# Kernel tuning notes

Measured on AMD Instinct MI355X. Metric: run time of the kernel, lower is better.

The kernel has to match this reference:

```python
import jax, jax.numpy as jnp
import numpy as np

MAX_SEQ_LEN = 128
H = 512
B = 256
S = 128
VOCAB = MAX_SEQ_LEN + 2
SOS = MAX_SEQ_LEN  # start token index in embedding table


def _lstm_cell(x, h, c, w_ih, w_hh, b):
    # PyTorch gate order: i, f, g, o
    z = x @ w_ih.T + h @ w_hh.T + b
    i, f, g, o = jnp.split(z, 4, axis=-1)
    c = jax.nn.sigmoid(f) * c + jax.nn.sigmoid(i) * jnp.tanh(g)
    h = jax.nn.sigmoid(o) * jnp.tanh(c)
    return h, c


def _run_layer(xs, w_ih, w_hh, b):
    nb = xs.shape[1]
    h0 = jnp.zeros((nb, H), xs.dtype)

    def step(carry, x):
        h, c = carry
        h, c = _lstm_cell(x, h, c, w_ih, w_hh, b)
        return (h, c), h

    (hT, cT), ys = jax.lax.scan(step, (h0, h0), xs)
    return ys, hT, cT


def _forward(l2_features, enc, dec, emb, fc1_w, fc1_b, fc2_w, fc2_b, fc3_w, mlp):
    xs = jnp.transpose(l2_features, (1, 0, 2))  # [S,B,F]
    hs, cs = [], []
    for (w_ih, w_hh, b) in enc:  # 3-layer encoder LSTM
        xs, hT, cT = _run_layer(xs, w_ih, w_hh, b)
        hs.append(hT)
        cs.append(cT)
    enc_outs = xs  # [S,B,H]
    h_stack = jnp.stack(hs)  # [3,B,H]
    c_stack = jnp.stack(cs)
    ot = enc_outs @ fc2_w.T + fc2_b  # [S,B,256], loop-invariant
    w1, b1, w2, b2, w3, b3 = mlp
    (dw_ih0, dw_hh0, db0), (dw_ih1, dw_hh1, db1), (dw_ih2, dw_hh2, db2) = dec
    nb = l2_features.shape[0]
    tok0 = jnp.full((nb,), SOS, dtype=jnp.int32)
    ctx0 = jnp.zeros((nb, H), l2_features.dtype)

    def dec_step(carry, _):
        h, c, ctx, tok = carry
        # dropout is identity in eval mode
        x = jnp.concatenate([emb[tok], ctx], axis=1)  # [B, 2H]
        h0, c0 = _lstm_cell(x, h[0], c[0], dw_ih0, dw_hh0, db0)
        h1, c1 = _lstm_cell(h0, h[1], c[1], dw_ih1, dw_hh1, db1)
        h2, c2 = _lstm_cell(h1, h[2], c[2], dw_ih2, dw_hh2, db2)
        ht = h2 @ fc1_w.T + fc1_b  # [B,256]
        scores = jnp.tanh(ot + ht[None]) @ fc3_w[0]  # [S,B]
        w = jax.nn.softmax(scores, axis=0)  # softmax over encoder time (dim 0)
        new_ctx = jnp.einsum('sb,sbd->bd', w, enc_outs)  # [B,H]
        hdd = jax.nn.relu(jnp.concatenate([h2, new_ctx], axis=1) @ w1.T + b1)
        hdd = jax.nn.relu(hdd @ w2.T + b2)
        out = hdd @ w3.T + b3  # [B, MAX_SEQ_LEN]
        new_tok = jnp.argmax(out, axis=-1).astype(jnp.int32)
        new_carry = (jnp.stack([h0, h1, h2]), jnp.stack([c0, c1, c2]), new_ctx, new_tok)
        return new_carry, out

    _, outs = jax.lax.scan(dec_step, (h_stack, c_stack, ctx0, tok0), None, length=MAX_SEQ_LEN)
    return outs  # [MAX_SEQ_LEN, B, MAX_SEQ_LEN]


def setup_inputs() -> dict:
    key = jax.random.key(0)
    ks = iter(jax.random.split(key, 40))

    def p(shape):
        return jax.random.normal(next(ks), shape, dtype=jnp.float32) * 0.05

    d = {"l2_features": jax.random.normal(next(ks), (B, S, MAX_SEQ_LEN), dtype=jnp.float32)}
    d["enc_w_ih0"] = p((4 * H, MAX_SEQ_LEN)); d["enc_w_hh0"] = p((4 * H, H)); d["enc_b0"] = p((4 * H,))
    d["enc_w_ih1"] = p((4 * H, H)); d["enc_w_hh1"] = p((4 * H, H)); d["enc_b1"] = p((4 * H,))
    d["enc_w_ih2"] = p((4 * H, H)); d["enc_w_hh2"] = p((4 * H, H)); d["enc_b2"] = p((4 * H,))
    d["dec_w_ih0"] = p((4 * H, 2 * H)); d["dec_w_hh0"] = p((4 * H, H)); d["dec_b0"] = p((4 * H,))
    d["dec_w_ih1"] = p((4 * H, H)); d["dec_w_hh1"] = p((4 * H, H)); d["dec_b1"] = p((4 * H,))
    d["dec_w_ih2"] = p((4 * H, H)); d["dec_w_hh2"] = p((4 * H, H)); d["dec_b2"] = p((4 * H,))
    d["emb"] = p((VOCAB, H))
    d["fc1_w"] = p((256, H)); d["fc1_b"] = p((256,))
    d["fc2_w"] = p((256, H)); d["fc2_b"] = p((256,))
    d["fc3_w"] = p((1, 256))
    d["mlp_w1"] = p((512, 1024)); d["mlp_b1"] = p((512,))
    d["mlp_w2"] = p((256, 512)); d["mlp_b2"] = p((256,))
    d["mlp_w3"] = p((MAX_SEQ_LEN, 256)); d["mlp_b3"] = p((MAX_SEQ_LEN,))
    return d


def reference(l2_features, enc_w_ih0, enc_w_hh0, enc_b0, enc_w_ih1, enc_w_hh1, enc_b1,
              enc_w_ih2, enc_w_hh2, enc_b2, dec_w_ih0, dec_w_hh0, dec_b0,
              dec_w_ih1, dec_w_hh1, dec_b1, dec_w_ih2, dec_w_hh2, dec_b2,
              emb, fc1_w, fc1_b, fc2_w, fc2_b, fc3_w,
              mlp_w1, mlp_b1, mlp_w2, mlp_b2, mlp_w3, mlp_b3):
    enc = ((enc_w_ih0, enc_w_hh0, enc_b0), (enc_w_ih1, enc_w_hh1, enc_b1), (enc_w_ih2, enc_w_hh2, enc_b2))
    dec = ((dec_w_ih0, dec_w_hh0, dec_b0), (dec_w_ih1, dec_w_hh1, dec_b1), (dec_w_ih2, dec_w_hh2, dec_b2))
    mlp = (mlp_w1, mlp_b1, mlp_w2, mlp_b2, mlp_w3, mlp_b3)
    return _forward(l2_features, enc, dec, emb, fc1_w, fc1_b, fc2_w, fc2_b, fc3_w, mlp)
```

## Files before the change

### kernel.cpp

```cpp
#include <hip/hip_runtime.h>

#define BB 256
#define SS 128
#define FDIM 128
#define HH 512
#define H4 2048
#define TDEC 128
#define SOS_TOK 128

typedef short short8 __attribute__((ext_vector_type(8)));
typedef float f32x4 __attribute__((ext_vector_type(4)));

__device__ __forceinline__ float sigf(float x){ return 1.0f/(1.0f+__expf(-x)); }
__device__ __forceinline__ float tanh_f(float x){ return 1.0f - 2.0f/(__expf(2.0f*x)+1.0f); }

__device__ __forceinline__ void split2(float x, unsigned& h, unsigned& m){
    union { float f; unsigned u; } a; a.f = x;
    h = (a.u + 0x7fffu + ((a.u>>16)&1u)) >> 16;
    union { unsigned u; float f; } hf; hf.u = h << 16;
    float r1 = x - hf.f;
    union { float f; unsigned u; } b; b.f = r1;
    m = (b.u + 0x7fffu + ((b.u>>16)&1u)) >> 16;
}

__device__ __forceinline__ void splitw8(float4 v, uint2& H, uint2& M){
    unsigned h0,m0,h1,m1,h2,m2,h3,m3;
    split2(v.x,h0,m0); split2(v.y,h1,m1); split2(v.z,h2,m2); split2(v.w,h3,m3);
    H.x = h0 | (h1<<16); H.y = h2 | (h3<<16);
    M.x = m0 | (m1<<16); M.y = m2 | (m3<<16);
}

__global__ void split_w(const float* __restrict__ srcA, int KA,
                        const float* __restrict__ srcB, int KB, int ilv,
                        unsigned short* __restrict__ ph, unsigned short* __restrict__ pm,
                        int N){
    int k = blockIdx.x*128 + threadIdx.x;
    int n = blockIdx.y;
    int K = KA + KB;
    if (k >= K) return;
    int row = ilv ? ((n&3)*512 + (n>>2)) : n;
    float w = (k < KA) ? srcA[(size_t)row*KA + k] : srcB[(size_t)row*KB + (k-KA)];
    unsigned h,m; split2(w,h,m);
    size_t off = (size_t)(k>>5)*((size_t)N*32) + (size_t)n*32
               + ((((k>>3)&3) ^ (n&3))<<3) + (k&7);
    ph[off]=(unsigned short)h; pm[off]=(unsigned short)m;
}

__global__ void repack_b(float* __restrict__ dst, const float* __restrict__ src){
    int id = blockIdx.x*256 + threadIdx.x;
    if (id >= 2048) return;
    int g = id & 3, q = id >> 2;
    dst[id] = src[g*512 + q];
}

__global__ void init_tok(int* __restrict__ tok){ tok[threadIdx.x] = SOS_TOK; }

#define MM3(AH,AM,BH,BM,C) \
  C = __builtin_amdgcn_mfma_f32_16x16x32_bf16(AH,BH,C,0,0,0); \
  C = __builtin_amdgcn_mfma_f32_16x16x32_bf16(AH,BM,C,0,0,0); \
  C = __builtin_amdgcn_mfma_f32_16x16x32_bf16(AM,BH,C,0,0,0);

template<int MODE>
__global__ __launch_bounds__(256) void mg(
    const float* __restrict__ A0, long a0B, long a0T,
    const float* __restrict__ A1, const float* __restrict__ A2,
    const int* __restrict__ tok, int ksh,
    const unsigned short* __restrict__ Wh, const unsigned short* __restrict__ Wm,
    int Nld, int Kc,
    const float* __restrict__ bias, int relu,
    float* __restrict__ out, long oB, long oT,
    const float* __restrict__ xz, float* __restrict__ c_io, float* __restrict__ seqo)
{
    __shared__ __align__(16) unsigned short sA[2][2][2048];
    __shared__ __align__(16) unsigned short sW[2][2][2048];
    const int tid = threadIdx.x;
    const int row0 = blockIdx.y * 64, col0 = blockIdx.x * 64;
    const int nk = Kc >> 5;

    f32x4 acc[2][2];
    acc[0][0] = (f32x4){0.f,0.f,0.f,0.f}; acc[0][1] = (f32x4){0.f,0.f,0.f,0.f};
    acc[1][0] = (f32x4){0.f,0.f,0.f,0.f}; acc[1][1] = (f32x4){0.f,0.f,0.f,0.f};

    const int sr = tid >> 2, q4 = tid & 3;
    const int gr = row0 + sr;
    long ro0;
    if (tok){ int rr = tok[gr & 255]; ro0 = (long)rr * a0B; }
    else ro0 = (long)(gr & 255)*a0B + (long)(gr >> 8)*a0T;
    const long ro1 = (long)gr * 512;
    const size_t wbase = (size_t)col0*32 + (size_t)tid*8;
    const int swz = sr & 3;
    const int b0 = sr*32 + (q4 & 1)*4;
    const int p0s = ((q4>>1) ^ swz) << 3;
    const int p1s = ((2 + (q4>>1)) ^ swz) << 3;

    float4 va0, va1; uint4 vw0, vw1;

    auto issue = [&](int kt){
        int kg = kt*32;
        int seg = kg >> ksh;
        const float* sp = (seg==0)? A0 : ((seg==1)? A1 : A2);
        long ro = (seg==0)? ro0 : ro1;
        int ko = kg & ((1<<ksh)-1);
        const float* p = sp + ro + ko + q4*4;
        va0 = *(const float4*)p;
        va1 = *(const float4*)(p + 16);
        size_t wi = (size_t)(kg>>5)*((size_t)Nld*32) + wbase;
        vw0 = *(const uint4*)(Wh + wi);
        vw1 = *(const uint4*)(Wm + wi);
    };
    auto commit = [&](int buf){
        uint2 H,M;
        splitw8(va0,H,M);
        *(uint2*)&sA[buf][0][b0 + p0s] = H;
        *(uint2*)&sA[buf][1][b0 + p0s] = M;
        splitw8(va1,H,M);
        *(uint2*)&sA[buf][0][b0 + p1s] = H;
        *(uint2*)&sA[buf][1][b0 + p1s] = M;
        *(uint4*)&sW[buf][0][tid*8] = vw0;
        *(uint4*)&sW[buf][1][tid*8] = vw1;
    };

    const int wid = tid >> 6, lane = tid & 63;
    const int wy = wid >> 1, wx = wid & 1;
    const int l15 = lane & 15, l4 = lane >> 4;
    const int offA = (wy*32 + l15)*32 + ((l4 ^ (l15&3))<<3);
    const int offB = (wx*32 + l15)*32 + ((l4 ^ (l15&3))<<3);

    auto compute = [&](int buf){
        short8 a0h = *(const short8*)&sA[buf][0][offA];
        short8 a0m = *(const short8*)&sA[buf][1][offA];
        short8 a1h = *(const short8*)&sA[buf][0][offA+512];
        short8 a1m = *(const short8*)&sA[buf][1][offA+512];
        short8 b0h = *(const short8*)&sW[buf][0][offB];
        short8 b0m = *(const short8*)&sW[buf][1][offB];
        short8 b1h = *(const short8*)&sW[buf][0][offB+512];
        short8 b1m = *(const short8*)&sW[buf][1][offB+512];
        MM3(a0h,a0m,b0h,b0m,acc[0][0])
        MM3(a0h,a0m,b1h,b1m,acc[0][1])
        MM3(a1h,a1m,b0h,b0m,acc[1][0])
        MM3(a1h,a1m,b1h,b1m,acc[1][1])
    };

    issue(0);
    commit(0);
    __syncthreads();
    int buf = 0;
    for (int kt=0; kt<nk; ++kt){
        bool more = (kt+1 < nk);
        if (more) issue(kt+1);
        compute(buf);
        if (more) commit(buf^1);
        __syncthreads();
        buf ^= 1;
    }

    if (MODE == 0){
        #pragma unroll
        for (int fa=0; fa<2; fa++){
            #pragma unroll
            for (int fb=0; fb<2; fb++){
                int gc = col0 + wx*32 + fb*16 + l15;
                float bv = bias ? bias[gc] : 0.0f;
                #pragma unroll
                for (int i=0;i<4;i++){
                    int r = row0 + wy*32 + fa*16 + l4*4 + i;
                    float v = acc[fa][fb][i] + bv;
                    if (relu) v = fmaxf(v, 0.0f);
                    out[(size_t)(r&255)*oB + (size_t)(r>>8)*oT + gc] = v;
                }
            }
        }
    } else {
        #pragma unroll
        for (int fa=0; fa<2; fa++){
            #pragma unroll
            for (int fb=0; fb<2; fb++){
                int gc = col0 + wx*32 + fb*16 + l15;
                int q = gc >> 2, g = gc & 3;
                float ab = xz ? 0.0f : bias[gc];
                #pragma unroll
                for (int i=0;i<4;i++){
                    int r = row0 + wy*32 + fa*16 + l4*4 + i;
                    float addv = xz ? xz[(size_t)r*2048 + gc] : ab;
                    float z = acc[fa][fb][i] + addv;
                    float x1 = __shfl_xor(z, 1);
                    float x2 = __shfl_xor(z, 2);
                    float x3 = __shfl_xor(z, 3);
                    float zi = (g==0)?z :(g==1)?x1:(g==2)?x2:x3;
                    float zf = (g==1)?z :(g==0)?x1:(g==3)?x2:x3;
                    float zg = (g==2)?z :(g==3)?x1:(g==0)?x2:x3;
                    float zo = (g==3)?z :(g==2)?x1:(g==1)?x2:x3;
                    float co = c_io[(size_t)r*512 + q];
                    float cn = sigf(zf)*co + sigf(zi)*tanh_f(zg);
                    float hn = sigf(zo)*tanh_f(cn);
                    if (g == 1) c_io[(size_t)r*512 + q] = cn;
                    else if (g == 0) seqo[(size_t)r*512 + q] = hn;
                }
            }
        }
    }
}

__global__ __launch_bounds__(256) void attn_fc1(
    const float* __restrict__ h2,
    const float* __restrict__ fc1w,
    const float* __restrict__ fc1b,
    const float* __restrict__ ot,
    const float* __restrict__ enc,
    const float* __restrict__ fc3,
    float* __restrict__ ctx)
{
    __shared__ float h2s[512], hts[256], f3s[256], wsm[SS];
    const int b = blockIdx.x, tid = threadIdx.x;
    h2s[tid]     = h2[(size_t)b*512 + tid];
    h2s[tid+256] = h2[(size_t)b*512 + tid + 256];
    f3s[tid] = fc3[tid];
    __syncthreads();
    {
        const float4* wr = (const float4*)(fc1w + (size_t)tid*512);
        float s0=0.f, s1=0.f;
        #pragma unroll 4
        for (int k4=0; k4<128; k4+=2){
            float4 w0 = wr[k4], w1 = wr[k4+1];
            float4 hh0 = *(const float4*)&h2s[k4*4];
            float4 hh1 = *(const float4*)&h2s[k4*4+4];
            s0 = fmaf(w0.x,hh0.x,fmaf(w0.y,hh0.y,fmaf(w0.z,hh0.z,fmaf(w0.w,hh0.w,s0))));
            s1 = fmaf(w1.x,hh1.x,fmaf(w1.y,hh1.y,fmaf(w1.z,hh1.z,fmaf(w1.w,hh1.w,s1))));
        }
        hts[tid] = s0 + s1 + fc1b[tid];
    }
    __syncthreads();
    const int wave = tid >> 6, lane = tid & 63;
    const float* otb = ot + (size_t)b*SS*256;
    for (int i=0;i<32;i++){
        int s = wave*32 + i;
        float4 o = *(const float4*)&otb[(size_t)s*256 + lane*4];
        int d0 = lane*4;
        float v = f3s[d0+0]*tanh_f(o.x + hts[d0+0])
                + f3s[d0+1]*tanh_f(o.y + hts[d0+1])
                + f3s[d0+2]*tanh_f(o.z + hts[d0+2])
                + f3s[d0+3]*tanh_f(o.w + hts[d0+3]);
        #pragma unroll
        for (int off=32; off; off>>=1) v += __shfl_xor(v, off);
        if (lane == 0) wsm[s] = v;
    }
    __syncthreads();
    if (tid < 64){
        float v0 = wsm[tid], v1 = wsm[tid+64];
        float m = fmaxf(v0, v1);
        #pragma unroll
        for (int off=32; off; off>>=1) m = fmaxf(m, __shfl_xor(m, off));
        float e0 = __expf(v0 - m), e1 = __expf(v1 - m);
        float ss = e0 + e1;
        #pragma unroll
        for (int off=32; off; off>>=1) ss += __shfl_xor(ss, off);
        float inv = 1.0f/ss;
        wsm[tid] = e0*inv; wsm[tid+64] = e1*inv;
    }
    __syncthreads();
    float a0=0.f, a1=0.f;
    const float* eb = enc + (size_t)b*HH;
    #pragma unroll 8
    for (int s=0;s<SS;s++){
        float w = wsm[s];
        const float* e = eb + (size_t)s*BB*HH;
        a0 = fmaf(w, e[tid],      a0);
        a1 = fmaf(w, e[tid+256],  a1);
    }
    ctx[(size_t)b*HH + tid]      = a0;
    ctx[(size_t)b*HH + tid+256]  = a1;
}

__global__ __launch_bounds__(128) void mlp3_argmax(
    const float* __restrict__ hdd2,
    const float* __restrict__ w3,
    const float* __restrict__ b3,
    float* __restrict__ outp,
    int* __restrict__ tok)
{
    __shared__ float hs[256], lg[128];
    const int b = blockIdx.x, tid = threadIdx.x;
    hs[tid]     = hdd2[(size_t)b*256 + tid];
    hs[tid+128] = hdd2[(size_t)b*256 + tid + 128];
    __syncthreads();
    const float4* wr = (const float4*)(w3 + (size_t)tid*256);
    float s0=0.f, s1=0.f;
    #pragma unroll 4
    for (int k4=0; k4<64; k4+=2){
        float4 w0 = wr[k4], w1 = wr[k4+1];
        float4 h0 = *(const float4*)&hs[k4*4];
        float4 h1 = *(const float4*)&hs[k4*4+4];
        s0 = fmaf(w0.x,h0.x,fmaf(w0.y,h0.y,fmaf(w0.z,h0.z,fmaf(w0.w,h0.w,s0))));
        s1 = fmaf(w1.x,h1.x,fmaf(w1.y,h1.y,fmaf(w1.z,h1.z,fmaf(w1.w,h1.w,s1))));
    }
    float v = s0 + s1 + b3[tid];
    outp[(size_t)b*128 + tid] = v;
    lg[tid] = v;
    __syncthreads();
    if (tid < 64){
        float v0 = lg[tid], v1 = lg[tid+64];
        float bv; int bi;
        if (v1 > v0){ bv = v1; bi = tid+64; } else { bv = v0; bi = tid; }
        #pragma unroll
        for (int off=32; off; off>>=1){
            float ov = __shfl_xor(bv, off);
            int   oi = __shfl_xor(bi, off);
            if (ov > bv || (ov == bv && oi < bi)){ bv = ov; bi = oi; }
        }
        if (tid == 0) tok[b] = bi;
    }
}

extern "C" void kernel_launch(void* const* d_in, const int* in_sizes, int n_in,
                              void* d_out, int out_size, void* d_ws, size_t ws_size,
                              hipStream_t stream)
{
    (void)in_sizes; (void)n_in; (void)out_size;
    const float* l2      = (const float*)d_in[0];
    const float* e_wih[3] = {(const float*)d_in[1],(const float*)d_in[4],(const float*)d_in[7]};
    const float* e_whh[3] = {(const float*)d_in[2],(const float*)d_in[5],(const float*)d_in[8]};
    const float* e_b[3]   = {(const float*)d_in[3],(const float*)d_in[6],(const float*)d_in[9]};
    const float* d_wih[3] = {(const float*)d_in[10],(const float*)d_in[13],(const float*)d_in[16]};
    const float* d_whh[3] = {(const float*)d_in[11],(const float*)d_in[14],(const float*)d_in[17]};
    const float* d_b[3]   = {(const float*)d_in[12],(const float*)d_in[15],(const float*)d_in[18]};
    const float* emb   = (const float*)d_in[19];
    const float* fc1_w = (const float*)d_in[20]; const float* fc1_b = (const float*)d_in[21];
    const float* fc2_w = (const float*)d_in[22]; const float* fc2_b = (const float*)d_in[23];
    const float* fc3_w = (const float*)d_in[24];
    const float* w1 = (const float*)d_in[25]; const float* b1 = (const float*)d_in[26];
    const float* w2 = (const float*)d_in[27]; const float* b2 = (const float*)d_in[28];
    const float* w3 = (const float*)d_in[29]; const float* b3 = (const float*)d_in[30];
    float* out = (float*)d_out;

    float* base = (float*)d_ws;
    size_t off = 0;
    auto alloc = [&](size_t n)->float*{ float* r = base + off; off = (off + n + 63) & ~(size_t)63; return r; };

    struct WSpec { const float* a; int ka; const float* b; int kb; int ilv; int n; };
    WSpec ws[13] = {
        {e_wih[0],128, nullptr,0, 1,2048}, {e_wih[1],512, nullptr,0, 1,2048}, {e_wih[2],512, nullptr,0, 1,2048},
        {e_whh[0],512, nullptr,0, 1,2048}, {e_whh[1],512, nullptr,0, 1,2048}, {e_whh[2],512, nullptr,0, 1,2048},
        {d_wih[0],1024, d_whh[0],512, 1,2048}, {d_wih[1],512, d_whh[1],512, 1,2048}, {d_wih[2],512, d_whh[2],512, 1,2048},
        {fc2_w,512, nullptr,0, 0,256},
        {w1,1024, nullptr,0, 0,512}, {w2,512, nullptr,0, 0,256}, {w3,256, nullptr,0, 0,128}
    };
    unsigned short* wp[13][2];
    for (int i=0;i<13;i++){
        size_t sz = (size_t)(ws[i].ka + ws[i].kb) * ws[i].n;
        float* blk = alloc(sz);
        wp[i][0] = (unsigned short*)blk;
        wp[i][1] = wp[i][0] + sz;
    }
    float* br_e[3]; for (int l=0;l<3;l++) br_e[l] = alloc(2048);
    float* br_d[3]; for (int l=0;l<3;l++) br_d[l] = alloc(2048);

    float* seq   = alloc((size_t)SS*BB*HH);
    float* ot    = alloc((size_t)BB*SS*256);
    float* zbuf  = alloc((size_t)BB*HH);
    float* cbuf[3]; for (int l=0;l<3;l++) cbuf[l] = alloc((size_t)BB*HH);
    float* hbuf[3][2];
    for (int l=0;l<3;l++) for (int p=0;p<2;p++) hbuf[l][p] = alloc((size_t)BB*HH);
    float* ctx  = alloc((size_t)BB*HH);
    float* hdd1 = alloc((size_t)BB*512);
    float* hdd2 = alloc((size_t)BB*256);
    int*   tok  = (int*)alloc(256);

    size_t remain = (ws_size/4 > off) ? (ws_size/4 - off) : 0;
    int CH = 4;
    if      (remain >= (size_t)32*BB*H4) CH = 32;
    else if (remain >= (size_t)16*BB*H4) CH = 16;
    else if (remain >= (size_t) 8*BB*H4) CH = 8;
    float* xz = base + off;

    for (int i=0;i<13;i++){
        int K = ws[i].ka + ws[i].kb;
        hipLaunchKernelGGL(split_w, dim3((K+127)/128, ws[i].n), dim3(128), 0, stream,
                           ws[i].a, ws[i].ka, ws[i].b, ws[i].kb, ws[i].ilv,
                           wp[i][0], wp[i][1], ws[i].n);
    }
    for (int l=0;l<3;l++){
        hipLaunchKernelGGL(repack_b, dim3(8), dim3(256), 0, stream, br_e[l], e_b[l]);
        hipLaunchKernelGGL(repack_b, dim3(8), dim3(256), 0, stream, br_d[l], d_b[l]);
    }
    hipMemsetAsync(zbuf, 0, (size_t)BB*HH*4, stream);
    for (int l=0;l<3;l++) hipMemsetAsync(cbuf[l], 0, (size_t)BB*HH*4, stream);
    hipMemsetAsync(ctx, 0, (size_t)BB*HH*4, stream);

    for (int l=0;l<3;l++){
        const int Kih = (l==0)? FDIM : HH;
        const int nch = SS / CH;
        for (int tc=0; tc<nch; tc++){
            const float* A0; long sB, sT;
            if (l == 0){ A0 = l2 + (size_t)tc*CH*FDIM; sB = (long)SS*FDIM; sT = FDIM; }
            else       { A0 = seq + (size_t)tc*CH*BB*HH; sB = HH; sT = (long)BB*HH; }
            hipLaunchKernelGGL((mg<0>), dim3(32, CH*4), dim3(256), 0, stream,
                A0, sB, sT, (const float*)nullptr, (const float*)nullptr, (const int*)nullptr, 30,
                wp[l][0], wp[l][1], 2048, Kih,
                br_e[l], 0, xz, (long)H4, (long)BB*H4,
                (const float*)nullptr, (float*)nullptr, (float*)nullptr);
            for (int ti=0; ti<CH; ti++){
                int t = tc*CH + ti;
                const float* hp = (t==0) ? zbuf : seq + (size_t)(t-1)*BB*HH;
                hipLaunchKernelGGL((mg<2>), dim3(32, 4), dim3(256), 0, stream,
                    hp, (long)HH, 0L, (const float*)nullptr, (const float*)nullptr, (const int*)nullptr, 30,
                    wp[3+l][0], wp[3+l][1], 2048, HH,
                    (const float*)nullptr, 0, (float*)nullptr, 0L, 0L,
                    xz + (size_t)ti*BB*H4, cbuf[l], seq + (size_t)t*BB*HH);
            }
        }
        hipMemcpyAsync(hbuf[l][0], seq + (size_t)(SS-1)*BB*HH, (size_t)BB*HH*4,
                       hipMemcpyDeviceToDevice, stream);
    }

    hipLaunchKernelGGL((mg<0>), dim3(4, 512), dim3(256), 0, stream,
        seq, (long)HH, (long)BB*HH, (const float*)nullptr, (const float*)nullptr, (const int*)nullptr, 30,
        wp[9][0], wp[9][1], 256, HH,
        fc2_b, 0, ot, (long)SS*256, 256L,
        (const float*)nullptr, (float*)nullptr, (float*)nullptr);

    hipLaunchKernelGGL(init_tok, dim3(1), dim3(256), 0, stream, tok);
    for (int t=0; t<TDEC; t++){
        const int p = t & 1;
        hipLaunchKernelGGL((mg<2>), dim3(32, 4), dim3(256), 0, stream,
            emb, (long)HH, 0L, ctx, hbuf[0][p], tok, 9,
            wp[6][0], wp[6][1], 2048, 3*HH,
            br_d[0], 0, (float*)nullptr, 0L, 0L,
            (const float*)nullptr, cbuf[0], hbuf[0][p^1]);
        hipLaunchKernelGGL((mg<2>), dim3(32, 4), dim3(256), 0, stream,
            hbuf[0][p^1], (long)HH, 0L, hbuf[1][p], (const float*)nullptr, (const int*)nullptr, 9,
            wp[7][0], wp[7][1], 2048, 2*HH,
            br_d[1], 0, (float*)nullptr, 0L, 0L,
            (const float*)nullptr, cbuf[1], hbuf[1][p^1]);
        hipLaunchKernelGGL((mg<2>), dim3(32, 4), dim3(256), 0, stream,
            hbuf[1][p^1], (long)HH, 0L, hbuf[2][p], (const float*)nullptr, (const int*)nullptr, 9,
            wp[8][0], wp[8][1], 2048, 2*HH,
            br_d[2], 0, (float*)nullptr, 0L, 0L,
            (const float*)nullptr, cbuf[2], hbuf[2][p^1]);
        hipLaunchKernelGGL(attn_fc1, dim3(BB), dim3(256), 0, stream,
            hbuf[2][p^1], fc1_w, fc1_b, ot, seq, fc3_w, ctx);
        hipLaunchKernelGGL((mg<0>), dim3(8, 4), dim3(256), 0, stream,
            hbuf[2][p^1], (long)HH, 0L, ctx, (const float*)nullptr, (const int*)nullptr, 9,
            wp[10][0], wp[10][1], 512, 2*HH,
            b1, 1, hdd1, 512L, 0L,
            (const float*)nullptr, (float*)nullptr, (float*)nullptr);
        hipLaunchKernelGGL((mg<0>), dim3(4, 4), dim3(256), 0, stream,
            hdd1, 512L, 0L, (const float*)nullptr, (const float*)nullptr, (const int*)nullptr, 30,
            wp[11][0], wp[11][1], 256, HH,
            b2, 1, hdd2, 256L, 0L,
            (const float*)nullptr, (float*)nullptr, (float*)nullptr);
        hipLaunchKernelGGL(mlp3_argmax, dim3(BB), dim3(128), 0, stream,
            hdd2, w3, b3, out + (size_t)t*BB*128, tok);
    }
}
```

Baseline: 32.81 ms.

## Replace per-step kernel launches with persistent encoder/decoder kernels using grid barriers

Replaces the many per-timestep launches (encoder chunked input GEMMs plus recurrent GEMMs, and seven kernels per decoder step) with two persistent 256-workgroup kernels that synchronise through a global atomic barrier. The encoder runs a wavefront over layers and time so that up to three layers' cells execute concurrently, and it fuses the input and hidden weights into a single K-concatenated GEMM. The decoder moves fc1 onto the split-bf16 MFMA path and runs attention, the MLP and argmax as phases inside one kernel. The goal is to remove launch overhead and serialisation on this latency-bound recurrence. In exchange it depends on all 256 workgroups being co-resident for the spin barrier to avoid deadlock, and many phases leave most workgroups idle.

```diff
diff --git a/kernel.cpp b/kernel.cpp
--- a/kernel.cpp
+++ b/kernel.cpp
@@ -7,9 +7,12 @@
 #define H4 2048
 #define TDEC 128
 #define SOS_TOK 128
+#define NWG 256
+#define SLOT 131072
 
 typedef short short8 __attribute__((ext_vector_type(8)));
 typedef float f32x4 __attribute__((ext_vector_type(4)));
+typedef unsigned short ushort_t;
 
 __device__ __forceinline__ float sigf(float x){ return 1.0f/(1.0f+__expf(-x)); }
 __device__ __forceinline__ float tanh_f(float x){ return 1.0f - 2.0f/(__expf(2.0f*x)+1.0f); }
@@ -32,8 +35,7 @@
 
 __global__ void split_w(const float* __restrict__ srcA, int KA,
                         const float* __restrict__ srcB, int KB, int ilv,
-                        unsigned short* __restrict__ ph, unsigned short* __restrict__ pm,
-                        int N){
+                        ushort_t* __restrict__ ph, ushort_t* __restrict__ pm, int N){
     int k = blockIdx.x*128 + threadIdx.x;
     int n = blockIdx.y;
     int K = KA + KB;
@@ -43,7 +45,7 @@
     unsigned h,m; split2(w,h,m);
     size_t off = (size_t)(k>>5)*((size_t)N*32) + (size_t)n*32
                + ((((k>>3)&3) ^ (n&3))<<3) + (k&7);
-    ph[off]=(unsigned short)h; pm[off]=(unsigned short)m;
+    ph[off]=(ushort_t)h; pm[off]=(ushort_t)m;
 }
 
 __global__ void repack_b(float* __restrict__ dst, const float* __restrict__ src){
@@ -53,58 +55,66 @@
     dst[id] = src[g*512 + q];
 }
 
-__global__ void init_tok(int* __restrict__ tok){ tok[threadIdx.x] = SOS_TOK; }
-
-#define MM3(AH,AM,BH,BM,C) \
-  C = __builtin_amdgcn_mfma_f32_16x16x32_bf16(AH,BH,C,0,0,0); \
-  C = __builtin_amdgcn_mfma_f32_16x16x32_bf16(AH,BM,C,0,0,0); \
-  C = __builtin_amdgcn_mfma_f32_16x16x32_bf16(AM,BH,C,0,0,0);
-
-template<int MODE>
-__global__ __launch_bounds__(256) void mg(
+__global__ void init_misc(int* bar){ if (threadIdx.x < 2) bar[threadIdx.x] = 0; }
+
+__device__ __forceinline__ void gbar(int* bar){
+    __syncthreads();
+    if (threadIdx.x == 0){
+        __threadfence();
+        int g = __hip_atomic_load(&bar[1], __ATOMIC_RELAXED, __HIP_MEMORY_SCOPE_AGENT);
+        int a = __hip_atomic_fetch_add(&bar[0], 1, __ATOMIC_ACQ_REL, __HIP_MEMORY_SCOPE_AGENT);
+        if (a == NWG-1){
+            __hip_atomic_store(&bar[0], 0, __ATOMIC_RELAXED, __HIP_MEMORY_SCOPE_AGENT);
+            __hip_atomic_fetch_add(&bar[1], 1, __ATOMIC_ACQ_REL, __HIP_MEMORY_SCOPE_AGENT);
+        } else {
+            while (__hip_atomic_load(&bar[1], __ATOMIC_ACQUIRE, __HIP_MEMORY_SCOPE_AGENT) == g)
+                __builtin_amdgcn_s_sleep(8);
+        }
+        __threadfence();
+    }
+    __syncthreads();
+}
+
+__device__ __forceinline__ void gtile(
+    ushort_t (&sA)[2][2][2048], ushort_t (&sW)[2][2][2048],
+    int row0, int col0,
     const float* __restrict__ A0, long a0B, long a0T,
     const float* __restrict__ A1, const float* __restrict__ A2,
-    const int* __restrict__ tok, int ksh,
-    const unsigned short* __restrict__ Wh, const unsigned short* __restrict__ Wm,
-    int Nld, int Kc,
-    const float* __restrict__ bias, int relu,
+    const int* __restrict__ tok,
+    int kx1, int kx2, int Kc,
+    const ushort_t* __restrict__ Wh, const ushort_t* __restrict__ Wm, int Nld,
+    const float* __restrict__ bias, int relu, int mode,
     float* __restrict__ out, long oB, long oT,
-    const float* __restrict__ xz, float* __restrict__ c_io, float* __restrict__ seqo)
+    float* __restrict__ c_io, float* __restrict__ seqo)
 {
-    __shared__ __align__(16) unsigned short sA[2][2][2048];
-    __shared__ __align__(16) unsigned short sW[2][2][2048];
     const int tid = threadIdx.x;
-    const int row0 = blockIdx.y * 64, col0 = blockIdx.x * 64;
     const int nk = Kc >> 5;
-
     f32x4 acc[2][2];
-    acc[0][0] = (f32x4){0.f,0.f,0.f,0.f}; acc[0][1] = (f32x4){0.f,0.f,0.f,0.f};
-    acc[1][0] = (f32x4){0.f,0.f,0.f,0.f}; acc[1][1] = (f32x4){0.f,0.f,0.f,0.f};
-
+    acc[0][0]=(f32x4){0.f,0.f,0.f,0.f}; acc[0][1]=(f32x4){0.f,0.f,0.f,0.f};
+    acc[1][0]=(f32x4){0.f,0.f,0.f,0.f}; acc[1][1]=(f32x4){0.f,0.f,0.f,0.f};
     const int sr = tid >> 2, q4 = tid & 3;
     const int gr = row0 + sr;
     long ro0;
-    if (tok){ int rr = tok[gr & 255]; ro0 = (long)rr * a0B; }
-    else ro0 = (long)(gr & 255)*a0B + (long)(gr >> 8)*a0T;
-    const long ro1 = (long)gr * 512;
+    if (tok) ro0 = (long)tok[gr & 255] * a0B;
+    else     ro0 = (long)(gr & 255)*a0B + (long)(gr >> 8)*a0T;
+    const long roh = (long)gr * 512;
     const size_t wbase = (size_t)col0*32 + (size_t)tid*8;
     const int swz = sr & 3;
     const int b0 = sr*32 + (q4 & 1)*4;
     const int p0s = ((q4>>1) ^ swz) << 3;
     const int p1s = ((2 + (q4>>1)) ^ swz) << 3;
-
     float4 va0, va1; uint4 vw0, vw1;
 
     auto issue = [&](int kt){
         int kg = kt*32;
-        int seg = kg >> ksh;
-        const float* sp = (seg==0)? A0 : ((seg==1)? A1 : A2);
-        long ro = (seg==0)? ro0 : ro1;
-        int ko = kg & ((1<<ksh)-1);
-        const float* p = sp + ro + ko + q4*4;
+        const float* sp; long ro; int kb;
+        if (kg < kx1){ sp=A0; ro=ro0; kb=kg; }
+        else if (kg < kx2){ sp=A1; ro=roh; kb=kg-kx1; }
+        else { sp=A2; ro=roh; kb=kg-kx2; }
+        const float* p = sp + ro + kb + q4*4;
         va0 = *(const float4*)p;
         va1 = *(const float4*)(p + 16);
-        size_t wi = (size_t)(kg>>5)*((size_t)Nld*32) + wbase;
+        size_t wi = (size_t)kt*((size_t)Nld*32) + wbase;
         vw0 = *(const uint4*)(Wh + wi);
         vw1 = *(const uint4*)(Wm + wi);
     };
@@ -135,10 +145,18 @@
         short8 b0m = *(const short8*)&sW[buf][1][offB];
         short8 b1h = *(const short8*)&sW[buf][0][offB+512];
         short8 b1m = *(const short8*)&sW[buf][1][offB+512];
-        MM3(a0h,a0m,b0h,b0m,acc[0][0])
-        MM3(a0h,a0m,b1h,b1m,acc[0][1])
-        MM3(a1h,a1m,b0h,b0m,acc[1][0])
-        MM3(a1h,a1m,b1h,b1m,acc[1][1])
+        acc[0][0] = __builtin_amdgcn_mfma_f32_16x16x32_bf16(a0h,b0h,acc[0][0],0,0,0);
+        acc[0][0] = __builtin_amdgcn_mfma_f32_16x16x32_bf16(a0h,b0m,acc[0][0],0,0,0);
+        acc[0][0] = __builtin_amdgcn_mfma_f32_16x16x32_bf16(a0m,b0h,acc[0][0],0,0,0);
+        acc[0][1] = __builtin_amdgcn_mfma_f32_16x16x32_bf16(a0h,b1h,acc[0][1],0,0,0);
+        acc[0][1] = __builtin_amdgcn_mfma_f32_16x16x32_bf16(a0h,b1m,acc[0][1],0,0,0);
+        acc[0][1] = __builtin_amdgcn_mfma_f32_16x16x32_bf16(a0m,b1h,acc[0][1],0,0,0);
+        acc[1][0] = __builtin_amdgcn_mfma_f32_16x16x32_bf16(a1h,b0h,acc[1][0],0,0,0);
+        acc[1][0] = __builtin_amdgcn_mfma_f32_16x16x32_bf16(a1h,b0m,acc[1][0],0,0,0);
+        acc[1][0] = __builtin_amdgcn_mfma_f32_16x16x32_bf16(a1m,b0h,acc[1][0],0,0,0);
+        acc[1][1] = __builtin_amdgcn_mfma_f32_16x16x32_bf16(a1h,b1h,acc[1][1],0,0,0);
+        acc[1][1] = __builtin_amdgcn_mfma_f32_16x16x32_bf16(a1h,b1m,acc[1][1],0,0,0);
+        acc[1][1] = __builtin_amdgcn_mfma_f32_16x16x32_bf16(a1m,b1h,acc[1][1],0,0,0);
     };
 
     issue(0);
@@ -154,7 +172,7 @@
         buf ^= 1;
     }
 
-    if (MODE == 0){
+    if (mode == 0){
         #pragma unroll
         for (int fa=0; fa<2; fa++){
             #pragma unroll
@@ -177,12 +195,11 @@
             for (int fb=0; fb<2; fb++){
                 int gc = col0 + wx*32 + fb*16 + l15;
                 int q = gc >> 2, g = gc & 3;
-                float ab = xz ? 0.0f : bias[gc];
+                float ab = bias[gc];
                 #pragma unroll
                 for (int i=0;i<4;i++){
                     int r = row0 + wy*32 + fa*16 + l4*4 + i;
-                    float addv = xz ? xz[(size_t)r*2048 + gc] : ab;
-                    float z = acc[fa][fb][i] + addv;
+                    float z = acc[fa][fb][i] + ab;
                     float x1 = __shfl_xor(z, 1);
                     float x2 = __shfl_xor(z, 2);
                     float x3 = __shfl_xor(z, 3);
@@ -201,113 +218,208 @@
     }
 }
 
-__global__ __launch_bounds__(256) void attn_fc1(
-    const float* __restrict__ h2,
-    const float* __restrict__ fc1w,
-    const float* __restrict__ fc1b,
-    const float* __restrict__ ot,
-    const float* __restrict__ enc,
-    const float* __restrict__ fc3,
-    float* __restrict__ ctx)
+__global__ __launch_bounds__(256) void gk(
+    const float* __restrict__ A0, long a0B, long a0T,
+    const ushort_t* __restrict__ Wh, const ushort_t* __restrict__ Wm, int Nld, int Kc,
+    const float* __restrict__ bias, float* __restrict__ out, long oB, long oT)
 {
-    __shared__ float h2s[512], hts[256], f3s[256], wsm[SS];
-    const int b = blockIdx.x, tid = threadIdx.x;
-    h2s[tid]     = h2[(size_t)b*512 + tid];
-    h2s[tid+256] = h2[(size_t)b*512 + tid + 256];
-    f3s[tid] = fc3[tid];
-    __syncthreads();
+    __shared__ __align__(16) ushort_t sA[2][2][2048];
+    __shared__ __align__(16) ushort_t sW[2][2][2048];
+    gtile(sA, sW, blockIdx.y*64, blockIdx.x*64,
+          A0, a0B, a0T, nullptr, nullptr, nullptr,
+          Kc, Kc, Kc, Wh, Wm, Nld, bias, 0, 0, out, oB, oT, nullptr, nullptr);
+}
+
+struct EncArgs {
+    const float* l2;
+    const ushort_t* Wh[3]; const ushort_t* Wm[3];
+    const float* bias[3];
+    float* bufraw; float* cst; int* bar;
+};
+
+__global__ __launch_bounds__(256) void enc_persist(EncArgs P){
+    __shared__ __align__(16) ushort_t sA[2][2][2048];
+    __shared__ __align__(16) ushort_t sW[2][2][2048];
+    const int wg = blockIdx.x, tid = threadIdx.x;
     {
-        const float4* wr = (const float4*)(fc1w + (size_t)tid*512);
-        float s0=0.f, s1=0.f;
-        #pragma unroll 4
-        for (int k4=0; k4<128; k4+=2){
-            float4 w0 = wr[k4], w1 = wr[k4+1];
-            float4 hh0 = *(const float4*)&h2s[k4*4];
-            float4 hh1 = *(const float4*)&h2s[k4*4+4];
-            s0 = fmaf(w0.x,hh0.x,fmaf(w0.y,hh0.y,fmaf(w0.z,hh0.z,fmaf(w0.w,hh0.w,s0))));
-            s1 = fmaf(w1.x,hh1.x,fmaf(w1.y,hh1.y,fmaf(w1.z,hh1.z,fmaf(w1.w,hh1.w,s1))));
-        }
-        hts[tid] = s0 + s1 + fc1b[tid];
-    }
-    __syncthreads();
-    const int wave = tid >> 6, lane = tid & 63;
-    const float* otb = ot + (size_t)b*SS*256;
-    for (int i=0;i<32;i++){
-        int s = wave*32 + i;
-        float4 o = *(const float4*)&otb[(size_t)s*256 + lane*4];
-        int d0 = lane*4;
-        float v = f3s[d0+0]*tanh_f(o.x + hts[d0+0])
-                + f3s[d0+1]*tanh_f(o.y + hts[d0+1])
-                + f3s[d0+2]*tanh_f(o.z + hts[d0+2])
-                + f3s[d0+3]*tanh_f(o.w + hts[d0+3]);
-        #pragma unroll
-        for (int off=32; off; off>>=1) v += __shfl_xor(v, off);
-        if (lane == 0) wsm[s] = v;
-    }
-    __syncthreads();
-    if (tid < 64){
-        float v0 = wsm[tid], v1 = wsm[tid+64];
-        float m = fmaxf(v0, v1);
-        #pragma unroll
-        for (int off=32; off; off>>=1) m = fmaxf(m, __shfl_xor(m, off));
-        float e0 = __expf(v0 - m), e1 = __expf(v1 - m);
-        float ss = e0 + e1;
-        #pragma unroll
-        for (int off=32; off; off>>=1) ss += __shfl_xor(ss, off);
-        float inv = 1.0f/ss;
-        wsm[tid] = e0*inv; wsm[tid+64] = e1*inv;
-    }
-    __syncthreads();
-    float a0=0.f, a1=0.f;
-    const float* eb = enc + (size_t)b*HH;
-    #pragma unroll 8
-    for (int s=0;s<SS;s++){
-        float w = wsm[s];
-        const float* e = eb + (size_t)s*BB*HH;
-        a0 = fmaf(w, e[tid],      a0);
-        a1 = fmaf(w, e[tid+256],  a1);
-    }
-    ctx[(size_t)b*HH + tid]      = a0;
-    ctx[(size_t)b*HH + tid+256]  = a1;
-}
-
-__global__ __launch_bounds__(128) void mlp3_argmax(
-    const float* __restrict__ hdd2,
-    const float* __restrict__ w3,
-    const float* __restrict__ b3,
-    float* __restrict__ outp,
-    int* __restrict__ tok)
-{
-    __shared__ float hs[256], lg[128];
-    const int b = blockIdx.x, tid = threadIdx.x;
-    hs[tid]     = hdd2[(size_t)b*256 + tid];
-    hs[tid+128] = hdd2[(size_t)b*256 + tid + 128];
-    __syncthreads();
-    const float4* wr = (const float4*)(w3 + (size_t)tid*256);
-    float s0=0.f, s1=0.f;
-    #pragma unroll 4
-    for (int k4=0; k4<64; k4+=2){
-        float4 w0 = wr[k4], w1 = wr[k4+1];
-        float4 h0 = *(const float4*)&hs[k4*4];
-        float4 h1 = *(const float4*)&hs[k4*4+4];
-        s0 = fmaf(w0.x,h0.x,fmaf(w0.y,h0.y,fmaf(w0.z,h0.z,fmaf(w0.w,h0.w,s0))));
-        s1 = fmaf(w1.x,h1.x,fmaf(w1.y,h1.y,fmaf(w1.z,h1.z,fmaf(w1.w,h1.w,s1))));
-    }
-    float v = s0 + s1 + b3[tid];
-    outp[(size_t)b*128 + tid] = v;
-    lg[tid] = v;
-    __syncthreads();
-    if (tid < 64){
-        float v0 = lg[tid], v1 = lg[tid+64];
-        float bv; int bi;
-        if (v1 > v0){ bv = v1; bi = tid+64; } else { bv = v0; bi = tid; }
-        #pragma unroll
-        for (int off=32; off; off>>=1){
-            float ov = __shfl_xor(bv, off);
-            int   oi = __shfl_xor(bi, off);
-            if (ov > bv || (ov == bv && oi < bi)){ bv = ov; bi = oi; }
-        }
-        if (tid == 0) tok[b] = bi;
+        float4 z = {0.f,0.f,0.f,0.f};
+        int id = wg*256 + tid;
+        float4* b4 = (float4*)P.bufraw;
+        float4* c4 = (float4*)P.cst;
+        for (int i=id; i<3*SLOT/4; i+=65536){ b4[i] = z; c4[i] = z; }
+    }
+    gbar(P.bar);
+    for (int tau=0; tau<130; ++tau){
+        int lmin = (tau > 127) ? (tau - 127) : 0;
+        int lmax = (tau < 2) ? tau : 2;
+        int ntask = (lmax - lmin + 1) * 128;
+        for (int task = wg; task < ntask; task += NWG){
+            int l = lmin + (task >> 7);
+            int s = tau - l;
+            int tt = task & 127;
+            int row0 = (tt & 3)*64, col0 = (tt >> 2)*64;
+            const float* A0; long a0B; int kx1, Kc;
+            if (l == 0){ A0 = P.l2 + (size_t)s*FDIM; a0B = (long)SS*FDIM; kx1 = 128; Kc = 640; }
+            else { A0 = P.bufraw + (size_t)(s+3-l+1)*SLOT; a0B = 512; kx1 = 512; Kc = 1024; }
+            const float* A1 = P.bufraw + (size_t)(s+1-l+1)*SLOT;
+            float* seqo = P.bufraw + (size_t)(s+2-l+1)*SLOT;
+            float* cio = P.cst + (size_t)l*SLOT;
+            gtile(sA, sW, row0, col0,
+                  A0, a0B, 0L, A1, nullptr, nullptr,
+                  kx1, Kc, Kc,
+                  P.Wh[l], P.Wm[l], 2048,
+                  P.bias[l], 0, 2,
+                  nullptr, 0L, 0L, cio, seqo);
+        }
+        gbar(P.bar);
+    }
+}
+
+struct DecArgs {
+    const float* emb; const float* fc3;
+    const ushort_t* Wh[7]; const ushort_t* Wm[7];
+    const float* bias[7];
+    float* bufraw; float* cst;
+    float* h00; float* h01; float* h10; float* h11; float* h20; float* h21;
+    float* ctx; float* ht; float* hdd1; float* hdd2;
+    float* ot; float* outp; int* tok; int* bar;
+};
+
+__global__ __launch_bounds__(256) void dec_persist(DecArgs P){
+    __shared__ __align__(16) ushort_t sA[2][2][2048];
+    __shared__ __align__(16) ushort_t sW[2][2][2048];
+    __shared__ float hts[256], f3s[256], wsm[SS], lgs[128];
+    const int wg = blockIdx.x, tid = threadIdx.x;
+    float* hp[3][2] = {{P.h00,P.h01},{P.h10,P.h11},{P.h20,P.h21}};
+    const float* enc = P.bufraw + SLOT;
+    {
+        int id = wg*256 + tid;
+        for (int l=0;l<3;l++){
+            const float4* src = (const float4*)(P.bufraw + (size_t)(129-l+1)*SLOT);
+            float4* dst = (float4*)hp[l][0];
+            for (int i=id; i<SLOT/4; i+=65536) dst[i] = src[i];
+        }
+        float4 z = {0.f,0.f,0.f,0.f};
+        float4* c4 = (float4*)P.ctx;
+        for (int i=id; i<SLOT/4; i+=65536) c4[i] = z;
+        if (id < 256) P.tok[id] = SOS_TOK;
+    }
+    gbar(P.bar);
+
+    for (int t=0; t<TDEC; ++t){
+        const int p = t & 1;
+        for (int task=wg; task<128; task+=NWG){
+            int row0=(task&3)*64, col0=(task>>2)*64;
+            gtile(sA,sW,row0,col0, P.emb,512L,0L, P.ctx, hp[0][p], P.tok,
+                  512,1024,1536, P.Wh[0],P.Wm[0],2048, P.bias[0],0,2,
+                  nullptr,0L,0L, P.cst, hp[0][p^1]);
+        }
+        gbar(P.bar);
+        for (int task=wg; task<128; task+=NWG){
+            int row0=(task&3)*64, col0=(task>>2)*64;
+            gtile(sA,sW,row0,col0, hp[0][p^1],512L,0L, hp[1][p], nullptr, nullptr,
+                  512,1024,1024, P.Wh[1],P.Wm[1],2048, P.bias[1],0,2,
+                  nullptr,0L,0L, P.cst+SLOT, hp[1][p^1]);
+        }
+        gbar(P.bar);
+        for (int task=wg; task<128; task+=NWG){
+            int row0=(task&3)*64, col0=(task>>2)*64;
+            gtile(sA,sW,row0,col0, hp[1][p^1],512L,0L, hp[2][p], nullptr, nullptr,
+                  512,1024,1024, P.Wh[2],P.Wm[2],2048, P.bias[2],0,2,
+                  nullptr,0L,0L, P.cst+2*SLOT, hp[2][p^1]);
+        }
+        gbar(P.bar);
+        for (int task=wg; task<16; task+=NWG){
+            int row0=(task&3)*64, col0=(task>>2)*64;
+            gtile(sA,sW,row0,col0, hp[2][p^1],512L,0L, nullptr,nullptr,nullptr,
+                  512,512,512, P.Wh[3],P.Wm[3],256, P.bias[3],0,0,
+                  P.ht,256L,0L, nullptr,nullptr);
+        }
+        gbar(P.bar);
+        {
+            int b = wg;
+            hts[tid] = P.ht[(size_t)b*256 + tid];
+            f3s[tid] = P.fc3[tid];
+            __syncthreads();
+            int wave = tid >> 6, lane = tid & 63;
+            const float* otb = P.ot + (size_t)b*SS*256;
+            for (int i=0;i<32;i++){
+                int s = wave*32 + i;
+                float4 o = *(const float4*)&otb[(size_t)s*256 + lane*4];
+                int d0 = lane*4;
+                float v = f3s[d0+0]*tanh_f(o.x + hts[d0+0])
+                        + f3s[d0+1]*tanh_f(o.y + hts[d0+1])
+                        + f3s[d0+2]*tanh_f(o.z + hts[d0+2])
+                        + f3s[d0+3]*tanh_f(o.w + hts[d0+3]);
+                #pragma unroll
+                for (int off=32; off; off>>=1) v += __shfl_xor(v, off);
+                if (lane == 0) wsm[s] = v;
+            }
+            __syncthreads();
+            if (tid < 64){
+                float v0 = wsm[tid], v1 = wsm[tid+64];
+                float m = fmaxf(v0, v1);
+                #pragma unroll
+                for (int off=32; off; off>>=1) m = fmaxf(m, __shfl_xor(m, off));
+                float e0 = __expf(v0 - m), e1 = __expf(v1 - m);
+                float ss = e0 + e1;
+                #pragma unroll
+                for (int off=32; off; off>>=1) ss += __shfl_xor(ss, off);
+                float inv = 1.0f/ss;
+                wsm[tid] = e0*inv; wsm[tid+64] = e1*inv;
+            }
+            __syncthreads();
+            float a0=0.f, a1=0.f;
+            const float* eb = enc + (size_t)b*HH;
+            #pragma unroll 8
+            for (int s=0;s<SS;s++){
+                float w = wsm[s];
+                const float* e = eb + (size_t)s*BB*HH;
+                a0 = fmaf(w, e[tid],     a0);
+                a1 = fmaf(w, e[tid+256], a1);
+            }
+            P.ctx[(size_t)b*HH + tid]     = a0;
+            P.ctx[(size_t)b*HH + tid+256] = a1;
+        }
+        gbar(P.bar);
+        for (int task=wg; task<32; task+=NWG){
+            int row0=(task&3)*64, col0=(task>>2)*64;
+            gtile(sA,sW,row0,col0, hp[2][p^1],512L,0L, P.ctx, nullptr, nullptr,
+                  512,1024,1024, P.Wh[4],P.Wm[4],512, P.bias[4],1,0,
+                  P.hdd1,512L,0L, nullptr,nullptr);
+        }
+        gbar(P.bar);
+        for (int task=wg; task<16; task+=NWG){
+            int row0=(task&3)*64, col0=(task>>2)*64;
+            gtile(sA,sW,row0,col0, P.hdd1,512L,0L, nullptr,nullptr,nullptr,
+                  512,512,512, P.Wh[5],P.Wm[5],256, P.bias[5],1,0,
+                  P.hdd2,256L,0L, nullptr,nullptr);
+        }
+        gbar(P.bar);
+        float* lgp = P.outp + (size_t)t*BB*128;
+        for (int task=wg; task<8; task+=NWG){
+            int row0=(task&3)*64, col0=(task>>2)*64;
+            gtile(sA,sW,row0,col0, P.hdd2,256L,0L, nullptr,nullptr,nullptr,
+                  256,256,256, P.Wh[6],P.Wm[6],128, P.bias[6],0,0,
+                  lgp,128L,0L, nullptr,nullptr);
+        }
+        gbar(P.bar);
+        if (wg < 64){
+            int r = wg*4 + (tid>>6), lane = tid & 63;
+            const float* lr_ = lgp + (size_t)r*128;
+            float v0 = lr_[lane], v1 = lr_[lane+64];
+            float bv; int bi;
+            if (v1 > v0){ bv=v1; bi=lane+64; } else { bv=v0; bi=lane; }
+            #pragma unroll
+            for (int off=32; off; off>>=1){
+                float ov = __shfl_xor(bv, off);
+                int   oi = __shfl_xor(bi, off);
+                if (ov > bv || (ov == bv && oi < bi)){ bv=ov; bi=oi; }
+            }
+            if (lane == 0) P.tok[r] = bi;
+        }
+        gbar(P.bar);
+        (void)lgs;
     }
 }
 
@@ -315,7 +427,7 @@
                               void* d_out, int out_size, void* d_ws, size_t ws_size,
                               hipStream_t stream)
 {
-    (void)in_sizes; (void)n_in; (void)out_size;
+    (void)in_sizes; (void)n_in; (void)out_size; (void)ws_size;
     const float* l2      = (const float*)d_in[0];
     const float* e_wih[3] = {(const float*)d_in[1],(const float*)d_in[4],(const float*)d_in[7]};
     const float* e_whh[3] = {(const float*)d_in[2],(const float*)d_in[5],(const float*)d_in[8]};
@@ -337,42 +449,42 @@
     auto alloc = [&](size_t n)->float*{ float* r = base + off; off = (off + n + 63) & ~(size_t)63; return r; };
 
     struct WSpec { const float* a; int ka; const float* b; int kb; int ilv; int n; };
-    WSpec ws[13] = {
-        {e_wih[0],128, nullptr,0, 1,2048}, {e_wih[1],512, nullptr,0, 1,2048}, {e_wih[2],512, nullptr,0, 1,2048},
-        {e_whh[0],512, nullptr,0, 1,2048}, {e_whh[1],512, nullptr,0, 1,2048}, {e_whh[2],512, nullptr,0, 1,2048},
-        {d_wih[0],1024, d_whh[0],512, 1,2048}, {d_wih[1],512, d_whh[1],512, 1,2048}, {d_wih[2],512, d_whh[2],512, 1,2048},
+    WSpec ws[11] = {
+        {e_wih[0],128, e_whh[0],512, 1,2048},
+        {e_wih[1],512, e_whh[1],512, 1,2048},
+        {e_wih[2],512, e_whh[2],512, 1,2048},
+        {d_wih[0],1024, d_whh[0],512, 1,2048},
+        {d_wih[1],512, d_whh[1],512, 1,2048},
+        {d_wih[2],512, d_whh[2],512, 1,2048},
+        {fc1_w,512, nullptr,0, 0,256},
         {fc2_w,512, nullptr,0, 0,256},
-        {w1,1024, nullptr,0, 0,512}, {w2,512, nullptr,0, 0,256}, {w3,256, nullptr,0, 0,128}
+        {w1,1024, nullptr,0, 0,512},
+        {w2,512, nullptr,0, 0,256},
+        {w3,256, nullptr,0, 0,128}
     };
-    unsigned short* wp[13][2];
-    for (int i=0;i<13;i++){
+    ushort_t* wp[11][2];
+    for (int i=0;i<11;i++){
         size_t sz = (size_t)(ws[i].ka + ws[i].kb) * ws[i].n;
         float* blk = alloc(sz);
-        wp[i][0] = (unsigned short*)blk;
+        wp[i][0] = (ushort_t*)blk;
         wp[i][1] = wp[i][0] + sz;
     }
     float* br_e[3]; for (int l=0;l<3;l++) br_e[l] = alloc(2048);
     float* br_d[3]; for (int l=0;l<3;l++) br_d[l] = alloc(2048);
 
-    float* seq   = alloc((size_t)SS*BB*HH);
-    float* ot    = alloc((size_t)BB*SS*256);
-    float* zbuf  = alloc((size_t)BB*HH);
-    float* cbuf[3]; for (int l=0;l<3;l++) cbuf[l] = alloc((size_t)BB*HH);
-    float* hbuf[3][2];
-    for (int l=0;l<3;l++) for (int p=0;p<2;p++) hbuf[l][p] = alloc((size_t)BB*HH);
-    float* ctx  = alloc((size_t)BB*HH);
-    float* hdd1 = alloc((size_t)BB*512);
-    float* hdd2 = alloc((size_t)BB*256);
-    int*   tok  = (int*)alloc(256);
-
-    size_t remain = (ws_size/4 > off) ? (ws_size/4 - off) : 0;
-    int CH = 4;
-    if      (remain >= (size_t)32*BB*H4) CH = 32;
-    else if (remain >= (size_t)16*BB*H4) CH = 16;
-    else if (remain >= (size_t) 8*BB*H4) CH = 8;
-    float* xz = base + off;
-
-    for (int i=0;i<13;i++){
+    float* bufraw = alloc((size_t)131*SLOT);
+    float* ot     = alloc((size_t)BB*SS*256);
+    float* cst    = alloc((size_t)3*SLOT);
+    float* hb     = alloc((size_t)6*SLOT);
+    float* ctx    = alloc((size_t)SLOT);
+    float* ht     = alloc((size_t)BB*256);
+    float* hdd1   = alloc((size_t)BB*512);
+    float* hdd2   = alloc((size_t)BB*256);
+    int*   tok    = (int*)alloc(256);
+    int*   bar    = (int*)alloc(64);
+
+    hipLaunchKernelGGL(init_misc, dim3(1), dim3(64), 0, stream, bar);
+    for (int i=0;i<11;i++){
         int K = ws[i].ka + ws[i].kb;
         hipLaunchKernelGGL(split_w, dim3((K+127)/128, ws[i].n), dim3(128), 0, stream,
                            ws[i].a, ws[i].ka, ws[i].b, ws[i].kb, ws[i].ilv,
@@ -382,73 +494,32 @@
         hipLaunchKernelGGL(repack_b, dim3(8), dim3(256), 0, stream, br_e[l], e_b[l]);
         hipLaunchKernelGGL(repack_b, dim3(8), dim3(256), 0, stream, br_d[l], d_b[l]);
     }
-    hipMemsetAsync(zbuf, 0, (size_t)BB*HH*4, stream);
-    for (int l=0;l<3;l++) hipMemsetAsync(cbuf[l], 0, (size_t)BB*HH*4, stream);
-    hipMemsetAsync(ctx, 0, (size_t)BB*HH*4, stream);
-
-    for (int l=0;l<3;l++){
-        const int Kih = (l==0)? FDIM : HH;
-        const int nch = SS / CH;
-        for (int tc=0; tc<nch; tc++){
-            const float* A0; long sB, sT;
-            if (l == 0){ A0 = l2 + (size_t)tc*CH*FDIM; sB = (long)SS*FDIM; sT = FDIM; }
-            else       { A0 = seq + (size_t)tc*CH*BB*HH; sB = HH; sT = (long)BB*HH; }
-            hipLaunchKernelGGL((mg<0>), dim3(32, CH*4), dim3(256), 0, stream,
-                A0, sB, sT, (const float*)nullptr, (const float*)nullptr, (const int*)nullptr, 30,
-                wp[l][0], wp[l][1], 2048, Kih,
-                br_e[l], 0, xz, (long)H4, (long)BB*H4,
-                (const float*)nullptr, (float*)nullptr, (float*)nullptr);
-            for (int ti=0; ti<CH; ti++){
-                int t = tc*CH + ti;
-                const float* hp = (t==0) ? zbuf : seq + (size_t)(t-1)*BB*HH;
-                hipLaunchKernelGGL((mg<2>), dim3(32, 4), dim3(256), 0, stream,
-                    hp, (long)HH, 0L, (const float*)nullptr, (const float*)nullptr, (const int*)nullptr, 30,
-                    wp[3+l][0], wp[3+l][1], 2048, HH,
-                    (const float*)nullptr, 0, (float*)nullptr, 0L, 0L,
-                    xz + (size_t)ti*BB*H4, cbuf[l], seq + (size_t)t*BB*HH);
-            }
-        }
-        hipMemcpyAsync(hbuf[l][0], seq + (size_t)(SS-1)*BB*HH, (size_t)BB*HH*4,
-                       hipMemcpyDeviceToDevice, stream);
-    }
-
-    hipLaunchKernelGGL((mg<0>), dim3(4, 512), dim3(256), 0, stream,
-        seq, (long)HH, (long)BB*HH, (const float*)nullptr, (const float*)nullptr, (const int*)nullptr, 30,
-        wp[9][0], wp[9][1], 256, HH,
-        fc2_b, 0, ot, (long)SS*256, 256L,
-        (const float*)nullptr, (float*)nullptr, (float*)nullptr);
-
-    hipLaunchKernelGGL(init_tok, dim3(1), dim3(256), 0, stream, tok);
-    for (int t=0; t<TDEC; t++){
-        const int p = t & 1;
-        hipLaunchKernelGGL((mg<2>), dim3(32, 4), dim3(256), 0, stream,
-            emb, (long)HH, 0L, ctx, hbuf[0][p], tok, 9,
-            wp[6][0], wp[6][1], 2048, 3*HH,
-            br_d[0], 0, (float*)nullptr, 0L, 0L,
-            (const float*)nullptr, cbuf[0], hbuf[0][p^1]);
-        hipLaunchKernelGGL((mg<2>), dim3(32, 4), dim3(256), 0, stream,
-            hbuf[0][p^1], (long)HH, 0L, hbuf[1][p], (const float*)nullptr, (const int*)nullptr, 9,
-            wp[7][0], wp[7][1], 2048, 2*HH,
-            br_d[1], 0, (float*)nullptr, 0L, 0L,
-            (const float*)nullptr, cbuf[1], hbuf[1][p^1]);
-        hipLaunchKernelGGL((mg<2>), dim3(32, 4), dim3(256), 0, stream,
-            hbuf[1][p^1], (long)HH, 0L, hbuf[2][p], (const float*)nullptr, (const int*)nullptr, 9,
-            wp[8][0], wp[8][1], 2048, 2*HH,
-            br_d[2], 0, (float*)nullptr, 0L, 0L,
-            (const float*)nullptr, cbuf[2], hbuf[2][p^1]);
-        hipLaunchKernelGGL(attn_fc1, dim3(BB), dim3(256), 0, stream,
-            hbuf[2][p^1], fc1_w, fc1_b, ot, seq, fc3_w, ctx);
-        hipLaunchKernelGGL((mg<0>), dim3(8, 4), dim3(256), 0, stream,
-            hbuf[2][p^1], (long)HH, 0L, ctx, (const float*)nullptr, (const int*)nullptr, 9,
-            wp[10][0], wp[10][1], 512, 2*HH,
-            b1, 1, hdd1, 512L, 0L,
-            (const float*)nullptr, (float*)nullptr, (float*)nullptr);
-        hipLaunchKernelGGL((mg<0>), dim3(4, 4), dim3(256), 0, stream,
-            hdd1, 512L, 0L, (const float*)nullptr, (const float*)nullptr, (const int*)nullptr, 30,
-            wp[11][0], wp[11][1], 256, HH,
-            b2, 1, hdd2, 256L, 0L,
-            (const float*)nullptr, (float*)nullptr, (float*)nullptr);
-        hipLaunchKernelGGL(mlp3_argmax, dim3(BB), dim3(128), 0, stream,
-            hdd2, w3, b3, out + (size_t)t*BB*128, tok);
-    }
-}
+
+    EncArgs ea;
+    ea.l2 = l2;
+    for (int l=0;l<3;l++){ ea.Wh[l]=wp[l][0]; ea.Wm[l]=wp[l][1]; ea.bias[l]=br_e[l]; }
+    ea.bufraw = bufraw; ea.cst = cst; ea.bar = bar;
+    hipLaunchKernelGGL(enc_persist, dim3(NWG), dim3(256), 0, stream, ea);
+
+    hipLaunchKernelGGL(gk, dim3(4, 512), dim3(256), 0, stream,
+        bufraw + SLOT, 512L, (long)SLOT, wp[7][0], wp[7][1], 256, 512,
+        fc2_b, ot, (long)SS*256, 256L);
+
+    DecArgs da;
+    da.emb = emb; da.fc3 = fc3_w;
+    for (int i=0;i<7;i++){ da.Wh[i]=wp[3+i==3?3:0][0]; }
+    da.Wh[0]=wp[3][0]; da.Wm[0]=wp[3][1]; da.bias[0]=br_d[0];
+    da.Wh[1]=wp[4][0]; da.Wm[1]=wp[4][1]; da.bias[1]=br_d[1];
+    da.Wh[2]=wp[5][0]; da.Wm[2]=wp[5][1]; da.bias[2]=br_d[2];
+    da.Wh[3]=wp[6][0]; da.Wm[3]=wp[6][1]; da.bias[3]=fc1_b;
+    da.Wh[4]=wp[8][0]; da.Wm[4]=wp[8][1]; da.bias[4]=b1;
+    da.Wh[5]=wp[9][0]; da.Wm[5]=wp[9][1]; da.bias[5]=b2;
+    da.Wh[6]=wp[10][0]; da.Wm[6]=wp[10][1]; da.bias[6]=b3;
+    da.bufraw = bufraw; da.cst = cst;
+    da.h00 = hb;        da.h01 = hb + SLOT;
+    da.h10 = hb + 2*SLOT; da.h11 = hb + 3*SLOT;
+    da.h20 = hb + 4*SLOT; da.h21 = hb + 5*SLOT;
+    da.ctx = ctx; da.ht = ht; da.hdd1 = hdd1; da.hdd2 = hdd2;
+    da.ot = ot; da.outp = out; da.tok = tok; da.bar = bar;
+    hipLaunchKernelGGL(dec_persist, dim3(NWG), dim3(256), 0, stream, da);
+}
```

After: 102.4 ms. 212% more time.
